# Optimization experiments

Measured on AMD Instinct MI355X. Metric: run time of the kernel, lower is better.

## Reference

```python
import jax, jax.numpy as jnp
import numpy as np

B, L, D, H, M = 2, 4096, 1024, 16, 256
DH = D // H
EPS = 1e-6
LN_EPS = 1e-5


def setup_inputs() -> dict:
    key = jax.random.key(0)
    ks = jax.random.split(key, 6)
    inp = {
        "x": jax.random.normal(ks[0], (B, L, D), jnp.float32),
        "Wq": jax.random.normal(ks[1], (D, D), jnp.float32) * (D ** -0.5),
        "Wk": jax.random.normal(ks[2], (D, D), jnp.float32) * (D ** -0.5),
        "Wv": jax.random.normal(ks[3], (D, D), jnp.float32) * (D ** -0.5),
        "Wo": jax.random.normal(ks[4], (D, D), jnp.float32) * (D ** -0.5),
        "proj": jax.random.normal(ks[5], (H, M, DH), jnp.float32),
        "ln_g": jnp.ones((D,), jnp.float32),
        "ln_b": jnp.zeros((D,), jnp.float32),
        "scale_factor": 2,
    }
    return inp


def _heads(t, W):
    b, l, _ = t.shape
    return (t @ W).reshape(b, l, H, DH).transpose(0, 2, 1, 3)  # bhld


def _favor_features(u, proj):
    # u: [B,H,L,DH] already scaled by d_head**-0.25; proj: [H,M,DH]
    dash = jnp.einsum("bhld,hmd->bhlm", u, proj)
    diag = 0.5 * jnp.sum(u * u, axis=-1, keepdims=True)  # [B,H,L,1]
    stab = jnp.max(dash, axis=-1, keepdims=True)
    return jnp.exp(dash - diag - stab) * (M ** -0.5)  # [B,H,L,M]


def reference(x, Wq, Wk, Wv, Wo, proj, ln_g, ln_b, scale_factor):
    b, l, d = x.shape
    # nearest-neighbor upsample along sequence (F.interpolate default mode)
    up = jnp.repeat(x, scale_factor, axis=1)  # [B, L*s, D]

    scale = DH ** -0.25
    q = _heads(up, Wq) * scale   # [B,H,Lq,DH]
    k = _heads(x, Wk) * scale    # [B,H,L,DH]
    v = _heads(x, Wv)            # [B,H,L,DH]

    qf = _favor_features(q, proj)  # [B,H,Lq,M]
    kf = _favor_features(k, proj)  # [B,H,L,M]

    kv = jnp.einsum("bhlm,bhld->bhmd", kf, v)          # [B,H,M,DH]
    k_sum = jnp.sum(kf, axis=2)                          # [B,H,M]
    z = 1.0 / (jnp.einsum("bhlm,bhm->bhl", qf, k_sum) + EPS)
    attn = jnp.einsum("bhlm,bhmd->bhld", qf, kv) * z[..., None]

    lq = attn.shape[2]
    y = attn.transpose(0, 2, 1, 3).reshape(b, lq, d) @ Wo
    y = jax.nn.gelu(y, approximate=False)

    mu = jnp.mean(y, axis=-1, keepdims=True)
    var = jnp.mean((y - mu) ** 2, axis=-1, keepdims=True)
    return (y - mu) * jax.lax.rsqrt(var + LN_EPS) * ln_g + ln_b
```

## Files before the change

### kernel.cpp

```cpp
#include <hip/hip_runtime.h>

static constexpr int kB  = 2;
static constexpr int kL  = 4096;
static constexpr int kD  = 1024;
static constexpr int kH  = 16;
static constexpr int kDH = 64;
static constexpr int kM  = 256;
static constexpr int kN  = kB * kL;
static constexpr float kScale    = 0.35355339059327373f;
static constexpr float kInvSqrtM = 0.0625f;
static constexpr float kEps   = 1e-6f;
static constexpr float kLnEps = 1e-5f;

typedef __attribute__((ext_vector_type(8))) short short8;
typedef __attribute__((ext_vector_type(4))) float f32x4;

__device__ __forceinline__ float bf2f(unsigned short h) {
  union { unsigned int u; float f; } c;
  c.u = ((unsigned int)h) << 16;
  return c.f;
}
__device__ __forceinline__ unsigned short f2bf(float f) {
  union { float f; unsigned int u; } c;
  c.f = f;
  unsigned int u = c.u;
  u += 0x7fffu + ((u >> 16) & 1u);
  return (unsigned short)(u >> 16);
}

__device__ __forceinline__ void gload_lds16(const unsigned short* g,
                                            unsigned short* l) {
  __builtin_amdgcn_global_load_lds(
      (const __attribute__((address_space(1))) unsigned int*)g,
      (__attribute__((address_space(3))) unsigned int*)l, 16, 0, 0);
}

__global__ __launch_bounds__(256) void cast_bf16_kernel(
    const float* __restrict__ in, unsigned short* __restrict__ out)
{
  const int i = blockIdx.x * 256 + threadIdx.x;
  float4 v = ((const float4*)in)[i];
  ushort4 o;
  o.x = f2bf(v.x); o.y = f2bf(v.y); o.z = f2bf(v.z); o.w = f2bf(v.w);
  ((ushort4*)out)[i] = o;
}

__global__ __launch_bounds__(256) void transpose_cast_kernel(
    const float* __restrict__ W, unsigned short* __restrict__ WT)
{
  __shared__ float tile[32][33];
  const int n0 = blockIdx.x * 32, k0 = blockIdx.y * 32;
  const int t = threadIdx.x, kk = t >> 5, nn = t & 31;
#pragma unroll
  for (int i = 0; i < 4; ++i)
    tile[kk + i * 8][nn] = W[(size_t)(k0 + kk + i * 8) * kD + n0 + nn];
  __syncthreads();
#pragma unroll
  for (int i = 0; i < 4; ++i)
    WT[(size_t)(n0 + kk + i * 8) * kD + k0 + nn] = f2bf(tile[nn][kk + i * 8]);
}

template <int OUT_MODE>
__global__ __launch_bounds__(256) void gemm_mfma(
    const unsigned short* __restrict__ A, const unsigned short* __restrict__ BT,
    void* __restrict__ Cout, float alpha)
{
  __shared__ unsigned short As[128 * 32];
  __shared__ unsigned short Bs[128 * 32];
  __shared__ unsigned short Tbuf[OUT_MODE == 2 ? 64 * 136 : 1];
  const int tid = threadIdx.x, lane = tid & 63, w = tid >> 6;
  const int q = lane >> 4, c = lane & 15;
  const int wr = (w >> 1) * 64, wc = (w & 1) * 64;
  const int row0 = blockIdx.y * 128, col0 = blockIdx.x * 128;
  const int lrow = lane >> 2, lcol = (lane & 3) * 8;

  f32x4 acc[4][4];
#pragma unroll
  for (int i = 0; i < 4; ++i)
#pragma unroll
    for (int j = 0; j < 4; ++j) acc[i][j] = (f32x4)0.f;

  for (int k0 = 0; k0 < kD; k0 += 32) {
#pragma unroll
    for (int i = 0; i < 2; ++i) {
      const int r0 = w * 32 + i * 16;
      gload_lds16(&A[(size_t)(row0 + r0 + lrow) * kD + k0 + lcol], &As[r0 * 32]);
      gload_lds16(&BT[(size_t)(col0 + r0 + lrow) * kD + k0 + lcol], &Bs[r0 * 32]);
    }
    __syncthreads();
    short8 av[4], bv[4];
#pragma unroll
    for (int i = 0; i < 4; ++i)
      av[i] = *(const short8*)&As[(wr + i * 16 + c) * 32 + q * 8];
#pragma unroll
    for (int j = 0; j < 4; ++j)
      bv[j] = *(const short8*)&Bs[(wc + j * 16 + c) * 32 + q * 8];
#pragma unroll
    for (int i = 0; i < 4; ++i)
#pragma unroll
      for (int j = 0; j < 4; ++j)
        acc[i][j] = __builtin_amdgcn_mfma_f32_16x16x32_bf16(
            av[i], bv[j], acc[i][j], 0, 0, 0);
    __syncthreads();
  }

  if (OUT_MODE != 2) {
#pragma unroll
    for (int i = 0; i < 4; ++i)
#pragma unroll
      for (int j = 0; j < 4; ++j)
#pragma unroll
        for (int r = 0; r < 4; ++r) {
          const int row = row0 + wr + i * 16 + q * 4 + r;
          const int col = col0 + wc + j * 16 + c;
          const float v = alpha * acc[i][j][r];
          if (OUT_MODE == 1)
            ((unsigned short*)Cout)[(size_t)row * kD + col] = f2bf(v);
          else
            ((float*)Cout)[(size_t)row * kD + col] = v;
        }
  } else {
    const int bq = row0 >> 12, l0 = row0 & 4095;
#pragma unroll
    for (int hh = 0; hh < 2; ++hh) {
      if ((w & 1) == hh) {
#pragma unroll
        for (int i = 0; i < 4; ++i)
#pragma unroll
          for (int j = 0; j < 4; ++j) {
            ushort4 o;
            o.x = f2bf(acc[i][j][0]); o.y = f2bf(acc[i][j][1]);
            o.z = f2bf(acc[i][j][2]); o.w = f2bf(acc[i][j][3]);
            *(ushort4*)&Tbuf[(j * 16 + c) * 136 + wr + i * 16 + q * 4] = o;
          }
      }
      __syncthreads();
      {
        const int dl = tid >> 2, seg = tid & 3;
        const size_t dst =
            ((size_t)(bq * 1024 + col0 + hh * 64 + dl)) * (size_t)kL +
            l0 + seg * 32;
        uint4* gp = (uint4*)((unsigned short*)Cout + dst);
        const unsigned short* sp = &Tbuf[dl * 136 + seg * 32];
#pragma unroll
        for (int u = 0; u < 4; ++u) gp[u] = *(const uint4*)&sp[u * 8];
      }
      __syncthreads();
    }
  }
}

template <int TRANS>
__global__ __launch_bounds__(256) void favor_mfma(
    const unsigned short* __restrict__ U, const unsigned short* __restrict__ projb,
    unsigned short* __restrict__ F)
{
  __shared__ unsigned short Us[128 * 72];
  __shared__ unsigned short Tbuf[TRANS ? 64 * 136 : 1];
  __shared__ float diagp[256];
  __shared__ float diag[128];
  const int bh = blockIdx.x, b = bh >> 4, h = bh & 15;
  const int l0 = blockIdx.y * 128;
  const int tid = threadIdx.x, lane = tid & 63, w = tid >> 6;
  const int q = lane >> 4, c = lane & 15;
  const int wr = w * 32;

#pragma unroll
  for (int it = 0; it < 4; ++it) {
    int idx = it * 256 + tid;
    int row = idx >> 3, col8 = idx & 7;
    *(uint4*)&Us[row * 72 + col8 * 8] =
        *(const uint4*)&U[((size_t)(b * kL + l0 + row)) * kD + h * kDH + col8 * 8];
  }
  __syncthreads();

  {
    int row = tid & 127, half = tid >> 7;
    const unsigned short* ur = &Us[row * 72 + half * 32];
    float s = 0.f;
#pragma unroll
    for (int d8 = 0; d8 < 4; ++d8) {
      uint4 raw = *(const uint4*)&ur[d8 * 8];
      const unsigned short* us = (const unsigned short*)&raw;
#pragma unroll
      for (int j = 0; j < 8; ++j) { float v = bf2f(us[j]); s = fmaf(v, v, s); }
    }
    diagp[half * 128 + row] = s;
  }

  f32x4 acc[2][16];
#pragma unroll
  for (int i = 0; i < 2; ++i)
#pragma unroll
    for (int j = 0; j < 16; ++j) acc[i][j] = (f32x4)0.f;

#pragma unroll
  for (int ks = 0; ks < 2; ++ks) {
    short8 av[2];
#pragma unroll
    for (int i = 0; i < 2; ++i)
      av[i] = *(const short8*)&Us[(wr + i * 16 + c) * 72 + ks * 32 + q * 8];
#pragma unroll
    for (int jb = 0; jb < 2; ++jb) {
      short8 bv[8];
#pragma unroll
      for (int jl = 0; jl < 8; ++jl)
        bv[jl] = *(const short8*)&projb[
            ((size_t)(h * kM + (jb * 8 + jl) * 16 + c)) * kDH + ks * 32 + q * 8];
#pragma unroll
      for (int jl = 0; jl < 8; ++jl)
#pragma unroll
        for (int i = 0; i < 2; ++i)
          acc[i][jb * 8 + jl] = __builtin_amdgcn_mfma_f32_16x16x32_bf16(
              av[i], bv[jl], acc[i][jb * 8 + jl], 0, 0, 0);
    }
  }

  __syncthreads();
  if (tid < 128) diag[tid] = 0.5f * (diagp[tid] + diagp[128 + tid]);
  __syncthreads();

#pragma unroll
  for (int i = 0; i < 2; ++i)
#pragma unroll
    for (int r = 0; r < 4; ++r) {
      const int lrow = wr + i * 16 + q * 4 + r;
      float mx = -3.4e38f;
#pragma unroll
      for (int j = 0; j < 16; ++j) mx = fmaxf(mx, acc[i][j][r]);
      mx = fmaxf(mx, __shfl_xor(mx, 1, 64));
      mx = fmaxf(mx, __shfl_xor(mx, 2, 64));
      mx = fmaxf(mx, __shfl_xor(mx, 4, 64));
      mx = fmaxf(mx, __shfl_xor(mx, 8, 64));
      const float base = diag[lrow] + mx;
      if (TRANS == 0) {
        const size_t gbase = ((size_t)bh * kL + (l0 + lrow)) * kM;
#pragma unroll
        for (int j = 0; j < 16; ++j)
          F[gbase + j * 16 + c] = f2bf(__expf(acc[i][j][r] - base) * kInvSqrtM);
      } else {
#pragma unroll
        for (int j = 0; j < 16; ++j)
          acc[i][j][r] = __expf(acc[i][j][r] - base) * kInvSqrtM;
      }
    }

  if (TRANS == 1) {
#pragma unroll
    for (int mc = 0; mc < 4; ++mc) {
      __syncthreads();
#pragma unroll
      for (int jl = 0; jl < 4; ++jl) {
        const int jj = mc * 4 + jl;
#pragma unroll
        for (int i = 0; i < 2; ++i) {
          ushort4 o;
          o.x = f2bf(acc[i][jj][0]); o.y = f2bf(acc[i][jj][1]);
          o.z = f2bf(acc[i][jj][2]); o.w = f2bf(acc[i][jj][3]);
          *(ushort4*)&Tbuf[(jl * 16 + c) * 136 + wr + i * 16 + q * 4] = o;
        }
      }
      __syncthreads();
#pragma unroll
      for (int it = 0; it < 4; ++it) {
        int idx = it * 256 + tid;
        int row = idx >> 4, col8 = idx & 15;
        *(uint4*)&F[((size_t)(bh * kM + mc * 64 + row)) * (size_t)kL +
                    l0 + col8 * 8] = *(const uint4*)&Tbuf[row * 136 + col8 * 8];
      }
    }
  }
}

__global__ __launch_bounds__(256) void kv_mfma(
    const unsigned short* __restrict__ KFT, const unsigned short* __restrict__ VT,
    float* __restrict__ KVP, float* __restrict__ KSP)
{
  __shared__ unsigned short As[128 * 40];
  __shared__ unsigned short Bs[64 * 40];
  const int bh = blockIdx.x, mtile = blockIdx.y, split = blockIdx.z;
  const int tid = threadIdx.x, lane = tid & 63, w = tid >> 6;
  const int q = lane >> 4, c = lane & 15;
  const int l0 = split * 512;
  const unsigned short* Abase = KFT + ((size_t)(bh * kM + mtile * 128)) * kL + l0;
  const unsigned short* Bbase = VT + ((size_t)(bh * kDH)) * kL + l0;

  f32x4 acc[2][4];
#pragma unroll
  for (int i = 0; i < 2; ++i)
#pragma unroll
    for (int j = 0; j < 4; ++j) acc[i][j] = (f32x4)0.f;
  float ksr[2] = {0.f, 0.f};

  for (int k0 = 0; k0 < 512; k0 += 32) {
    __syncthreads();
#pragma unroll
    for (int it = 0; it < 2; ++it) {
      int idx = it * 256 + tid;
      int row = idx >> 2, c8 = (idx & 3) * 8;
      *(uint4*)&As[row * 40 + c8] = *(const uint4*)&Abase[(size_t)row * kL + k0 + c8];
    }
    {
      int row = tid >> 2, c8 = (tid & 3) * 8;
      *(uint4*)&Bs[row * 40 + c8] = *(const uint4*)&Bbase[(size_t)row * kL + k0 + c8];
    }
    __syncthreads();
    short8 av[2], bv[4];
#pragma unroll
    for (int i = 0; i < 2; ++i) {
      av[i] = *(const short8*)&As[(w * 32 + i * 16 + c) * 40 + q * 8];
#pragma unroll
      for (int e = 0; e < 8; ++e) ksr[i] += bf2f((unsigned short)av[i][e]);
    }
#pragma unroll
    for (int j = 0; j < 4; ++j)
      bv[j] = *(const short8*)&Bs[(j * 16 + c) * 40 + q * 8];
#pragma unroll
    for (int i = 0; i < 2; ++i)
#pragma unroll
      for (int j = 0; j < 4; ++j)
        acc[i][j] = __builtin_amdgcn_mfma_f32_16x16x32_bf16(
            av[i], bv[j], acc[i][j], 0, 0, 0);
  }

  const int blk = (bh * 2 + mtile) * 8 + split;
  float* op = KVP + (size_t)blk * (128 * 64);
#pragma unroll
  for (int i = 0; i < 2; ++i)
#pragma unroll
    for (int j = 0; j < 4; ++j)
#pragma unroll
      for (int r = 0; r < 4; ++r)
        op[(w * 32 + i * 16 + q * 4 + r) * 64 + j * 16 + c] = acc[i][j][r];

#pragma unroll
  for (int i = 0; i < 2; ++i) {
    float s = ksr[i];
    s += __shfl_xor(s, 16, 64);
    s += __shfl_xor(s, 32, 64);
    if (q == 0) KSP[blk * 128 + w * 32 + i * 16 + c] = s;
  }
}

__global__ __launch_bounds__(256) void kv_reduce_kernel(
    const float* __restrict__ KVP, const float* __restrict__ KSP,
    unsigned short* __restrict__ KVT)
{
  const int blk = blockIdx.x;
  const int bh = blk / 80, n = blk - bh * 80;
  const int t = threadIdx.x;
  const int mt = t >> 7, ml = t & 127;
  float s = 0.f;
  if (n < 64) {
#pragma unroll
    for (int sp = 0; sp < 8; ++sp)
      s += KVP[((size_t)((bh * 2 + mt) * 8 + sp)) * (128 * 64) + ml * 64 + n];
  } else if (n == 64) {
#pragma unroll
    for (int sp = 0; sp < 8; ++sp)
      s += KSP[((bh * 2 + mt) * 8 + sp) * 128 + ml];
  }
  KVT[(size_t)bh * (80 * kM) + n * kM + t] = f2bf(s);
}

__global__ __launch_bounds__(256) void attn_mfma(
    const unsigned short* __restrict__ QF, const unsigned short* __restrict__ KVT,
    unsigned short* __restrict__ ATTN)
{
  __shared__ unsigned short kvs[80 * 264];
  __shared__ unsigned short qs[128 * 40];
  const int bh = blockIdx.x, b = bh >> 4, h = bh & 15;
  const int l0 = blockIdx.y * 128;
  const int tid = threadIdx.x, lane = tid & 63, w = tid >> 6;
  const int q = lane >> 4, c = lane & 15;
  const int trow = tid >> 2, tc8 = (tid & 3) * 8;

#pragma unroll
  for (int it = 0; it < 20; ++it) {
    int idx4 = it * 256 + tid;
    int row = idx4 >> 6, col4 = idx4 & 63;
    *(ushort4*)&kvs[row * 264 + col4 * 4] =
        *(const ushort4*)&KVT[(size_t)bh * (80 * kM) + row * kM + col4 * 4];
  }

  f32x4 acc[2][5];
#pragma unroll
  for (int i = 0; i < 2; ++i)
#pragma unroll
    for (int j = 0; j < 5; ++j) acc[i][j] = (f32x4)0.f;

  for (int kk = 0; kk < 8; ++kk) {
    __syncthreads();
#pragma unroll
    for (int i = 0; i < 2; ++i)
      *(uint4*)&qs[(trow + 64 * i) * 40 + tc8] =
          *(const uint4*)&QF[((size_t)bh * kL + (l0 + trow + 64 * i)) * kM +
                             kk * 32 + tc8];
    __syncthreads();
    short8 bv[5];
#pragma unroll
    for (int j = 0; j < 5; ++j)
      bv[j] = *(const short8*)&kvs[(j * 16 + c) * 264 + kk * 32 + q * 8];
#pragma unroll
    for (int i = 0; i < 2; ++i) {
      short8 av = *(const short8*)&qs[(w * 32 + i * 16 + c) * 40 + q * 8];
#pragma unroll
      for (int j = 0; j < 5; ++j)
        acc[i][j] = __builtin_amdgcn_mfma_f32_16x16x32_bf16(
            av, bv[j], acc[i][j], 0, 0, 0);
    }
  }

#pragma unroll
  for (int i = 0; i < 2; ++i)
#pragma unroll
    for (int r = 0; r < 4; ++r) {
      float den = __shfl(acc[i][4][r], (lane & 48));
      float z = 1.f / (den + kEps);
      const int row = l0 + w * 32 + i * 16 + q * 4 + r;
      const size_t base = ((size_t)(b * kL + row)) * kD + h * kDH;
#pragma unroll
      for (int j = 0; j < 4; ++j)
        ATTN[base + j * 16 + c] = f2bf(acc[i][j][r] * z);
    }
}

__global__ __launch_bounds__(256) void gelu_ln_kernel(
    const float* __restrict__ Y, const float* __restrict__ lng,
    const float* __restrict__ lnb, float* __restrict__ OUT)
{
  __shared__ float r1[4], r2[4];
  const int n = blockIdx.x;
  const int tid = threadIdx.x, lane = tid & 63, w = tid >> 6;

  float4 y4 = ((const float4*)(Y + (size_t)n * kD))[tid];
  float g0 = 0.5f * y4.x * (1.f + erff(y4.x * 0.70710678118654752f));
  float g1 = 0.5f * y4.y * (1.f + erff(y4.y * 0.70710678118654752f));
  float g2 = 0.5f * y4.z * (1.f + erff(y4.z * 0.70710678118654752f));
  float g3 = 0.5f * y4.w * (1.f + erff(y4.w * 0.70710678118654752f));

  float s  = (g0 + g1) + (g2 + g3);
  float ss = (g0 * g0 + g1 * g1) + (g2 * g2 + g3 * g3);
#pragma unroll
  for (int off = 32; off; off >>= 1) {
    s  += __shfl_xor(s, off, 64);
    ss += __shfl_xor(ss, off, 64);
  }
  if (lane == 0) { r1[w] = s; r2[w] = ss; }
  __syncthreads();
  s  = (r1[0] + r1[1]) + (r1[2] + r1[3]);
  ss = (r2[0] + r2[1]) + (r2[2] + r2[3]);
  float mu  = s * (1.f / (float)kD);
  float var = ss * (1.f / (float)kD) - mu * mu;
  float inv = rsqrtf(var + kLnEps);

  float4 gg = ((const float4*)lng)[tid];
  float4 bb = ((const float4*)lnb)[tid];
  float4 o;
  o.x = (g0 - mu) * inv * gg.x + bb.x;
  o.y = (g1 - mu) * inv * gg.y + bb.y;
  o.z = (g2 - mu) * inv * gg.z + bb.z;
  o.w = (g3 - mu) * inv * gg.w + bb.w;

  const int b = n >> 12, l = n & 4095;
  const int cc = tid * 4;
  size_t base = ((size_t)(b * 8192 + 2 * l)) * kD + cc;
  *(float4*)(OUT + base)      = o;
  *(float4*)(OUT + base + kD) = o;
}

extern "C" void kernel_launch(void* const* d_in, const int* in_sizes, int n_in,
                              void* d_out, int out_size, void* d_ws, size_t ws_size,
                              hipStream_t stream)
{
  (void)in_sizes; (void)n_in; (void)out_size; (void)ws_size;
  const float* x    = (const float*)d_in[0];
  const float* Wq   = (const float*)d_in[1];
  const float* Wk   = (const float*)d_in[2];
  const float* Wv   = (const float*)d_in[3];
  const float* Wo   = (const float*)d_in[4];
  const float* proj = (const float*)d_in[5];
  const float* lng  = (const float*)d_in[6];
  const float* lnb  = (const float*)d_in[7];
  float* out = (float*)d_out;

  char* ws = (char*)d_ws;
  const size_t MB = 1024 * 1024;
  unsigned short* xb  = (unsigned short*)(ws);
  unsigned short* WqT = (unsigned short*)(ws + 16 * MB);
  unsigned short* WkT = (unsigned short*)(ws + 18 * MB);
  unsigned short* WvT = (unsigned short*)(ws + 20 * MB);
  unsigned short* WoT = (unsigned short*)(ws + 22 * MB);
  unsigned short* Qb  = (unsigned short*)(ws + 24 * MB);
  unsigned short* Kb  = (unsigned short*)(ws + 40 * MB);
  unsigned short* VT  = (unsigned short*)(ws + 56 * MB);
  unsigned short* QF  = (unsigned short*)(ws + 72 * MB);
  unsigned short* KFT = (unsigned short*)(ws + 136 * MB);
  float* KSP          = (float*)(ws + 200 * MB);
  unsigned short* KVT = (unsigned short*)(ws + 201 * MB);
  unsigned short* projb = (unsigned short*)(ws + 203 * MB);
  float* KVP          = (float*)(ws + 24 * MB);
  unsigned short* ATTN = Kb;
  float* Y            = (float*)(ws + 72 * MB);

  cast_bf16_kernel<<<(kN * kD) / 1024, 256, 0, stream>>>(x, xb);
  cast_bf16_kernel<<<(kH * kM * kDH) / 1024, 256, 0, stream>>>(proj, projb);
  transpose_cast_kernel<<<dim3(32, 32), 256, 0, stream>>>(Wq, WqT);
  transpose_cast_kernel<<<dim3(32, 32), 256, 0, stream>>>(Wk, WkT);
  transpose_cast_kernel<<<dim3(32, 32), 256, 0, stream>>>(Wv, WvT);
  transpose_cast_kernel<<<dim3(32, 32), 256, 0, stream>>>(Wo, WoT);

  dim3 gg(8, 64);
  gemm_mfma<1><<<gg, 256, 0, stream>>>(xb, WkT, Kb, kScale);
  gemm_mfma<2><<<gg, 256, 0, stream>>>(xb, WvT, VT, 1.0f);
  gemm_mfma<1><<<gg, 256, 0, stream>>>(xb, WqT, Qb, kScale);

  favor_mfma<0><<<dim3(32, 32), 256, 0, stream>>>(Qb, projb, QF);
  favor_mfma<1><<<dim3(32, 32), 256, 0, stream>>>(Kb, projb, KFT);

  kv_mfma<<<dim3(32, 2, 8), 256, 0, stream>>>(KFT, VT, KVP, KSP);
  kv_reduce_kernel<<<32 * 80, 256, 0, stream>>>(KVP, KSP, KVT);

  attn_mfma<<<dim3(32, 32), 256, 0, stream>>>(QF, KVT, ATTN);

  gemm_mfma<0><<<gg, 256, 0, stream>>>(ATTN, WoT, Y, 1.0f);

  gelu_ln_kernel<<<kN, 256, 0, stream>>>(Y, lng, lnb, out);
}
```

Before: 389.4 us.

## Halve favor kernel row tile and drop LDS transpose for key features

The favor feature kernel now processes 64 rows per block instead of 128, so each wave holds one 16-row MFMA tile and half the accumulators, with a launch bound requesting higher occupancy and twice as many blocks. The transposed key-feature path no longer stages through an LDS buffer with extra barriers. It writes 4-element bf16 vectors straight to global memory in the transposed layout. This is meant to cut register pressure and barrier cost, at the price of narrower, less coalesced global stores and reloading projection rows for more blocks.

New measurement: 403.9 us. 1.04x slower.

```diff
diff --git a/kernel.cpp b/kernel.cpp
--- a/kernel.cpp
+++ b/kernel.cpp
@@ -151,22 +151,21 @@
 }
 
 template <int TRANS>
-__global__ __launch_bounds__(256) void favor_mfma(
+__global__ __launch_bounds__(256, 4) void favor_mfma(
     const unsigned short* __restrict__ U, const unsigned short* __restrict__ projb,
     unsigned short* __restrict__ F)
 {
-  __shared__ unsigned short Us[128 * 72];
-  __shared__ unsigned short Tbuf[TRANS ? 64 * 136 : 1];
-  __shared__ float diagp[256];
-  __shared__ float diag[128];
+  __shared__ unsigned short Us[64 * 72];
+  __shared__ float diagp[4][64];
+  __shared__ float diag[64];
   const int bh = blockIdx.x, b = bh >> 4, h = bh & 15;
-  const int l0 = blockIdx.y * 128;
+  const int l0 = blockIdx.y * 64;
   const int tid = threadIdx.x, lane = tid & 63, w = tid >> 6;
   const int q = lane >> 4, c = lane & 15;
-  const int wr = w * 32;
-
-#pragma unroll
-  for (int it = 0; it < 4; ++it) {
+  const int wrow = w * 16;
+
+#pragma unroll
+  for (int it = 0; it < 2; ++it) {
     int idx = it * 256 + tid;
     int row = idx >> 3, col8 = idx & 7;
     *(uint4*)&Us[row * 72 + col8 * 8] =
@@ -175,99 +174,77 @@
   __syncthreads();
 
   {
-    int row = tid & 127, half = tid >> 7;
-    const unsigned short* ur = &Us[row * 72 + half * 32];
+    int row = tid & 63, seg = tid >> 6;
+    const unsigned short* ur = &Us[row * 72 + seg * 16];
     float s = 0.f;
 #pragma unroll
-    for (int d8 = 0; d8 < 4; ++d8) {
+    for (int d8 = 0; d8 < 2; ++d8) {
       uint4 raw = *(const uint4*)&ur[d8 * 8];
       const unsigned short* us = (const unsigned short*)&raw;
 #pragma unroll
       for (int j = 0; j < 8; ++j) { float v = bf2f(us[j]); s = fmaf(v, v, s); }
     }
-    diagp[half * 128 + row] = s;
-  }
-
-  f32x4 acc[2][16];
-#pragma unroll
-  for (int i = 0; i < 2; ++i)
-#pragma unroll
-    for (int j = 0; j < 16; ++j) acc[i][j] = (f32x4)0.f;
+    diagp[seg][row] = s;
+  }
+  __syncthreads();
+  if (tid < 64)
+    diag[tid] = 0.5f * ((diagp[0][tid] + diagp[1][tid]) +
+                        (diagp[2][tid] + diagp[3][tid]));
+
+  f32x4 acc[16];
+#pragma unroll
+  for (int j = 0; j < 16; ++j) acc[j] = (f32x4)0.f;
 
 #pragma unroll
   for (int ks = 0; ks < 2; ++ks) {
-    short8 av[2];
-#pragma unroll
-    for (int i = 0; i < 2; ++i)
-      av[i] = *(const short8*)&Us[(wr + i * 16 + c) * 72 + ks * 32 + q * 8];
-#pragma unroll
-    for (int jb = 0; jb < 2; ++jb) {
-      short8 bv[8];
-#pragma unroll
-      for (int jl = 0; jl < 8; ++jl)
+    const short8 av = *(const short8*)&Us[(wrow + c) * 72 + ks * 32 + q * 8];
+#pragma unroll
+    for (int jb = 0; jb < 4; ++jb) {
+      short8 bv[4];
+#pragma unroll
+      for (int jl = 0; jl < 4; ++jl)
         bv[jl] = *(const short8*)&projb[
-            ((size_t)(h * kM + (jb * 8 + jl) * 16 + c)) * kDH + ks * 32 + q * 8];
-#pragma unroll
-      for (int jl = 0; jl < 8; ++jl)
-#pragma unroll
-        for (int i = 0; i < 2; ++i)
-          acc[i][jb * 8 + jl] = __builtin_amdgcn_mfma_f32_16x16x32_bf16(
-              av[i], bv[jl], acc[i][jb * 8 + jl], 0, 0, 0);
-    }
-  }
-
+            ((size_t)(h * kM + (jb * 4 + jl) * 16 + c)) * kDH + ks * 32 + q * 8];
+#pragma unroll
+      for (int jl = 0; jl < 4; ++jl)
+        acc[jb * 4 + jl] = __builtin_amdgcn_mfma_f32_16x16x32_bf16(
+            av, bv[jl], acc[jb * 4 + jl], 0, 0, 0);
+    }
+  }
   __syncthreads();
-  if (tid < 128) diag[tid] = 0.5f * (diagp[tid] + diagp[128 + tid]);
-  __syncthreads();
-
-#pragma unroll
-  for (int i = 0; i < 2; ++i)
+
+  float base_[4];
+#pragma unroll
+  for (int r = 0; r < 4; ++r) {
+    float mx = -3.4e38f;
+#pragma unroll
+    for (int j = 0; j < 16; ++j) mx = fmaxf(mx, acc[j][r]);
+    mx = fmaxf(mx, __shfl_xor(mx, 1, 64));
+    mx = fmaxf(mx, __shfl_xor(mx, 2, 64));
+    mx = fmaxf(mx, __shfl_xor(mx, 4, 64));
+    mx = fmaxf(mx, __shfl_xor(mx, 8, 64));
+    base_[r] = diag[wrow + q * 4 + r] + mx;
+  }
+
+  if (TRANS == 0) {
 #pragma unroll
     for (int r = 0; r < 4; ++r) {
-      const int lrow = wr + i * 16 + q * 4 + r;
-      float mx = -3.4e38f;
-#pragma unroll
-      for (int j = 0; j < 16; ++j) mx = fmaxf(mx, acc[i][j][r]);
-      mx = fmaxf(mx, __shfl_xor(mx, 1, 64));
-      mx = fmaxf(mx, __shfl_xor(mx, 2, 64));
-      mx = fmaxf(mx, __shfl_xor(mx, 4, 64));
-      mx = fmaxf(mx, __shfl_xor(mx, 8, 64));
-      const float base = diag[lrow] + mx;
-      if (TRANS == 0) {
-        const size_t gbase = ((size_t)bh * kL + (l0 + lrow)) * kM;
-#pragma unroll
-        for (int j = 0; j < 16; ++j)
-          F[gbase + j * 16 + c] = f2bf(__expf(acc[i][j][r] - base) * kInvSqrtM);
-      } else {
-#pragma unroll
-        for (int j = 0; j < 16; ++j)
-          acc[i][j][r] = __expf(acc[i][j][r] - base) * kInvSqrtM;
-      }
-    }
-
-  if (TRANS == 1) {
-#pragma unroll
-    for (int mc = 0; mc < 4; ++mc) {
-      __syncthreads();
-#pragma unroll
-      for (int jl = 0; jl < 4; ++jl) {
-        const int jj = mc * 4 + jl;
-#pragma unroll
-        for (int i = 0; i < 2; ++i) {
-          ushort4 o;
-          o.x = f2bf(acc[i][jj][0]); o.y = f2bf(acc[i][jj][1]);
-          o.z = f2bf(acc[i][jj][2]); o.w = f2bf(acc[i][jj][3]);
-          *(ushort4*)&Tbuf[(jl * 16 + c) * 136 + wr + i * 16 + q * 4] = o;
-        }
-      }
-      __syncthreads();
-#pragma unroll
-      for (int it = 0; it < 4; ++it) {
-        int idx = it * 256 + tid;
-        int row = idx >> 4, col8 = idx & 15;
-        *(uint4*)&F[((size_t)(bh * kM + mc * 64 + row)) * (size_t)kL +
-                    l0 + col8 * 8] = *(const uint4*)&Tbuf[row * 136 + col8 * 8];
-      }
+      const size_t gbase = ((size_t)bh * kL + (l0 + wrow + q * 4 + r)) * kM;
+#pragma unroll
+      for (int j = 0; j < 16; ++j)
+        F[gbase + j * 16 + c] =
+            f2bf(__expf(acc[j][r] - base_[r]) * kInvSqrtM);
+    }
+  } else {
+#pragma unroll
+    for (int j = 0; j < 16; ++j) {
+      ushort4 o;
+      o.x = f2bf(__expf(acc[j][0] - base_[0]) * kInvSqrtM);
+      o.y = f2bf(__expf(acc[j][1] - base_[1]) * kInvSqrtM);
+      o.z = f2bf(__expf(acc[j][2] - base_[2]) * kInvSqrtM);
+      o.w = f2bf(__expf(acc[j][3] - base_[3]) * kInvSqrtM);
+      *(ushort4*)&F[((size_t)(bh * kM + j * 16 + c)) * (size_t)kL +
+                    l0 + wrow + q * 4] = o;
     }
   }
 }
@@ -515,8 +492,8 @@
   gemm_mfma<2><<<gg, 256, 0, stream>>>(xb, WvT, VT, 1.0f);
   gemm_mfma<1><<<gg, 256, 0, stream>>>(xb, WqT, Qb, kScale);
 
-  favor_mfma<0><<<dim3(32, 32), 256, 0, stream>>>(Qb, projb, QF);
-  favor_mfma<1><<<dim3(32, 32), 256, 0, stream>>>(Kb, projb, KFT);
+  favor_mfma<0><<<dim3(32, 64), 256, 0, stream>>>(Qb, projb, QF);
+  favor_mfma<1><<<dim3(32, 64), 256, 0, stream>>>(Kb, projb, KFT);
 
   kv_mfma<<<dim3(32, 2, 8), 256, 0, stream>>>(KFT, VT, KVP, KSP);
   kv_reduce_kernel<<<32 * 80, 256, 0, stream>>>(KVP, KSP, KVT);
```

## Fuse query FAVOR feature computation into the attention kernel

Applied to the files above, without the earlier changes.

Query random features are now computed in LDS inside a new fused kernel that immediately multiplies them with the reduced KV/normalizer matrix. The large QF intermediate is no longer written to or read back from global memory. The key-side favor kernel becomes a dedicated transposed-output version, and launches are reordered with the workspace offsets compacted. The fused kernel reads KVT directly from global/L2 rather than staging it in LDS, and uses smaller 64-row tiles.

After: 387.9 us. About the same (-0.4%).

```diff
diff --git a/kernel.cpp b/kernel.cpp
--- a/kernel.cpp
+++ b/kernel.cpp
@@ -150,13 +150,12 @@
   }
 }
 
-template <int TRANS>
-__global__ __launch_bounds__(256) void favor_mfma(
+__global__ __launch_bounds__(256) void favor_k_mfma(
     const unsigned short* __restrict__ U, const unsigned short* __restrict__ projb,
     unsigned short* __restrict__ F)
 {
   __shared__ unsigned short Us[128 * 72];
-  __shared__ unsigned short Tbuf[TRANS ? 64 * 136 : 1];
+  __shared__ unsigned short Tbuf[64 * 136];
   __shared__ float diagp[256];
   __shared__ float diag[128];
   const int bh = blockIdx.x, b = bh >> 4, h = bh & 15;
@@ -233,42 +232,160 @@
       mx = fmaxf(mx, __shfl_xor(mx, 4, 64));
       mx = fmaxf(mx, __shfl_xor(mx, 8, 64));
       const float base = diag[lrow] + mx;
-      if (TRANS == 0) {
-        const size_t gbase = ((size_t)bh * kL + (l0 + lrow)) * kM;
-#pragma unroll
-        for (int j = 0; j < 16; ++j)
-          F[gbase + j * 16 + c] = f2bf(__expf(acc[i][j][r] - base) * kInvSqrtM);
-      } else {
-#pragma unroll
-        for (int j = 0; j < 16; ++j)
-          acc[i][j][r] = __expf(acc[i][j][r] - base) * kInvSqrtM;
+#pragma unroll
+      for (int j = 0; j < 16; ++j)
+        acc[i][j][r] = __expf(acc[i][j][r] - base) * kInvSqrtM;
+    }
+
+#pragma unroll
+  for (int mc = 0; mc < 4; ++mc) {
+    __syncthreads();
+#pragma unroll
+    for (int jl = 0; jl < 4; ++jl) {
+      const int jj = mc * 4 + jl;
+#pragma unroll
+      for (int i = 0; i < 2; ++i) {
+        ushort4 o;
+        o.x = f2bf(acc[i][jj][0]); o.y = f2bf(acc[i][jj][1]);
+        o.z = f2bf(acc[i][jj][2]); o.w = f2bf(acc[i][jj][3]);
+        *(ushort4*)&Tbuf[(jl * 16 + c) * 136 + wr + i * 16 + q * 4] = o;
       }
     }
-
-  if (TRANS == 1) {
-#pragma unroll
-    for (int mc = 0; mc < 4; ++mc) {
-      __syncthreads();
-#pragma unroll
-      for (int jl = 0; jl < 4; ++jl) {
-        const int jj = mc * 4 + jl;
-#pragma unroll
-        for (int i = 0; i < 2; ++i) {
-          ushort4 o;
-          o.x = f2bf(acc[i][jj][0]); o.y = f2bf(acc[i][jj][1]);
-          o.z = f2bf(acc[i][jj][2]); o.w = f2bf(acc[i][jj][3]);
-          *(ushort4*)&Tbuf[(jl * 16 + c) * 136 + wr + i * 16 + q * 4] = o;
-        }
-      }
-      __syncthreads();
-#pragma unroll
-      for (int it = 0; it < 4; ++it) {
-        int idx = it * 256 + tid;
-        int row = idx >> 4, col8 = idx & 15;
-        *(uint4*)&F[((size_t)(bh * kM + mc * 64 + row)) * (size_t)kL +
-                    l0 + col8 * 8] = *(const uint4*)&Tbuf[row * 136 + col8 * 8];
-      }
-    }
+    __syncthreads();
+#pragma unroll
+    for (int it = 0; it < 4; ++it) {
+      int idx = it * 256 + tid;
+      int row = idx >> 4, col8 = idx & 15;
+      *(uint4*)&F[((size_t)(bh * kM + mc * 64 + row)) * (size_t)kL +
+                  l0 + col8 * 8] = *(const uint4*)&Tbuf[row * 136 + col8 * 8];
+    }
+  }
+}
+
+__global__ __launch_bounds__(256, 3) void fused_qattn(
+    const unsigned short* __restrict__ Qb, const unsigned short* __restrict__ projb,
+    const unsigned short* __restrict__ KVT, unsigned short* __restrict__ ATTN)
+{
+  __shared__ unsigned short qs[64 * 72];
+  __shared__ unsigned short qfs[64 * 264];
+  __shared__ float diagp[4][64];
+  __shared__ float maxp[4][64];
+  __shared__ float basev[64];
+  const int bh = blockIdx.x, b = bh >> 4, h = bh & 15;
+  const int l0 = blockIdx.y * 64;
+  const int tid = threadIdx.x, lane = tid & 63, w = tid >> 6;
+  const int q = lane >> 4, c = lane & 15;
+
+#pragma unroll
+  for (int it = 0; it < 2; ++it) {
+    int idx = it * 256 + tid;
+    int row = idx >> 3, col8 = idx & 7;
+    *(uint4*)&qs[row * 72 + col8 * 8] =
+        *(const uint4*)&Qb[((size_t)(b * kL + l0 + row)) * kD + h * kDH + col8 * 8];
+  }
+  __syncthreads();
+
+  {
+    int row = tid & 63, seg = tid >> 6;
+    const unsigned short* ur = &qs[row * 72 + seg * 16];
+    float s = 0.f;
+#pragma unroll
+    for (int d8 = 0; d8 < 2; ++d8) {
+      uint4 raw = *(const uint4*)&ur[d8 * 8];
+      const unsigned short* us = (const unsigned short*)&raw;
+#pragma unroll
+      for (int j = 0; j < 8; ++j) { float v = bf2f(us[j]); s = fmaf(v, v, s); }
+    }
+    diagp[seg][row] = s;
+  }
+
+  f32x4 acc[4][4];
+#pragma unroll
+  for (int i = 0; i < 4; ++i)
+#pragma unroll
+    for (int j = 0; j < 4; ++j) acc[i][j] = (f32x4)0.f;
+
+#pragma unroll
+  for (int ks = 0; ks < 2; ++ks) {
+    short8 av[4], bv[4];
+#pragma unroll
+    for (int i = 0; i < 4; ++i)
+      av[i] = *(const short8*)&projb[
+          ((size_t)(h * kM + w * 64 + i * 16 + c)) * kDH + ks * 32 + q * 8];
+#pragma unroll
+    for (int j = 0; j < 4; ++j)
+      bv[j] = *(const short8*)&qs[(j * 16 + c) * 72 + ks * 32 + q * 8];
+#pragma unroll
+    for (int i = 0; i < 4; ++i)
+#pragma unroll
+      for (int j = 0; j < 4; ++j)
+        acc[i][j] = __builtin_amdgcn_mfma_f32_16x16x32_bf16(
+            av[i], bv[j], acc[i][j], 0, 0, 0);
+  }
+
+#pragma unroll
+  for (int j = 0; j < 4; ++j) {
+    float mx = -3.4e38f;
+#pragma unroll
+    for (int i = 0; i < 4; ++i)
+#pragma unroll
+      for (int r = 0; r < 4; ++r) mx = fmaxf(mx, acc[i][j][r]);
+    mx = fmaxf(mx, __shfl_xor(mx, 16, 64));
+    mx = fmaxf(mx, __shfl_xor(mx, 32, 64));
+    if (q == 0) maxp[w][j * 16 + c] = mx;
+  }
+  __syncthreads();
+  if (tid < 64) {
+    float d = 0.5f * ((diagp[0][tid] + diagp[1][tid]) +
+                      (diagp[2][tid] + diagp[3][tid]));
+    float m4 = fmaxf(fmaxf(maxp[0][tid], maxp[1][tid]),
+                     fmaxf(maxp[2][tid], maxp[3][tid]));
+    basev[tid] = d + m4;
+  }
+  __syncthreads();
+
+#pragma unroll
+  for (int j = 0; j < 4; ++j) {
+    const float bs = basev[j * 16 + c];
+#pragma unroll
+    for (int i = 0; i < 4; ++i) {
+      ushort4 o;
+      o.x = f2bf(__expf(acc[i][j][0] - bs) * kInvSqrtM);
+      o.y = f2bf(__expf(acc[i][j][1] - bs) * kInvSqrtM);
+      o.z = f2bf(__expf(acc[i][j][2] - bs) * kInvSqrtM);
+      o.w = f2bf(__expf(acc[i][j][3] - bs) * kInvSqrtM);
+      *(ushort4*)&qfs[(j * 16 + c) * 264 + w * 64 + i * 16 + q * 4] = o;
+    }
+  }
+  __syncthreads();
+
+  f32x4 acc2[5];
+#pragma unroll
+  for (int j = 0; j < 5; ++j) acc2[j] = (f32x4)0.f;
+
+#pragma unroll
+  for (int kk = 0; kk < 8; ++kk) {
+    short8 av2 = *(const short8*)&qfs[(w * 16 + c) * 264 + kk * 32 + q * 8];
+    short8 bv2[5];
+#pragma unroll
+    for (int j = 0; j < 5; ++j)
+      bv2[j] = *(const short8*)&KVT[
+          (size_t)bh * (80 * kM) + (j * 16 + c) * kM + kk * 32 + q * 8];
+#pragma unroll
+    for (int j = 0; j < 5; ++j)
+      acc2[j] = __builtin_amdgcn_mfma_f32_16x16x32_bf16(
+          av2, bv2[j], acc2[j], 0, 0, 0);
+  }
+
+#pragma unroll
+  for (int r = 0; r < 4; ++r) {
+    float den = __shfl(acc2[4][r], (lane & 48));
+    float z = 1.f / (den + kEps);
+    const int row = l0 + w * 16 + q * 4 + r;
+    const size_t base = ((size_t)(b * kL + row)) * kD + h * kDH;
+#pragma unroll
+    for (int j = 0; j < 4; ++j)
+      ATTN[base + j * 16 + c] = f2bf(acc2[j][r] * z);
   }
 }
 
@@ -361,68 +478,6 @@
       s += KSP[((bh * 2 + mt) * 8 + sp) * 128 + ml];
   }
   KVT[(size_t)bh * (80 * kM) + n * kM + t] = f2bf(s);
-}
-
-__global__ __launch_bounds__(256) void attn_mfma(
-    const unsigned short* __restrict__ QF, const unsigned short* __restrict__ KVT,
-    unsigned short* __restrict__ ATTN)
-{
-  __shared__ unsigned short kvs[80 * 264];
-  __shared__ unsigned short qs[128 * 40];
-  const int bh = blockIdx.x, b = bh >> 4, h = bh & 15;
-  const int l0 = blockIdx.y * 128;
-  const int tid = threadIdx.x, lane = tid & 63, w = tid >> 6;
-  const int q = lane >> 4, c = lane & 15;
-  const int trow = tid >> 2, tc8 = (tid & 3) * 8;
-
-#pragma unroll
-  for (int it = 0; it < 20; ++it) {
-    int idx4 = it * 256 + tid;
-    int row = idx4 >> 6, col4 = idx4 & 63;
-    *(ushort4*)&kvs[row * 264 + col4 * 4] =
-        *(const ushort4*)&KVT[(size_t)bh * (80 * kM) + row * kM + col4 * 4];
-  }
-
-  f32x4 acc[2][5];
-#pragma unroll
-  for (int i = 0; i < 2; ++i)
-#pragma unroll
-    for (int j = 0; j < 5; ++j) acc[i][j] = (f32x4)0.f;
-
-  for (int kk = 0; kk < 8; ++kk) {
-    __syncthreads();
-#pragma unroll
-    for (int i = 0; i < 2; ++i)
-      *(uint4*)&qs[(trow + 64 * i) * 40 + tc8] =
-          *(const uint4*)&QF[((size_t)bh * kL + (l0 + trow + 64 * i)) * kM +
-                             kk * 32 + tc8];
-    __syncthreads();
-    short8 bv[5];
-#pragma unroll
-    for (int j = 0; j < 5; ++j)
-      bv[j] = *(const short8*)&kvs[(j * 16 + c) * 264 + kk * 32 + q * 8];
-#pragma unroll
-    for (int i = 0; i < 2; ++i) {
-      short8 av = *(const short8*)&qs[(w * 32 + i * 16 + c) * 40 + q * 8];
-#pragma unroll
-      for (int j = 0; j < 5; ++j)
-        acc[i][j] = __builtin_amdgcn_mfma_f32_16x16x32_bf16(
-            av, bv[j], acc[i][j], 0, 0, 0);
-    }
-  }
-
-#pragma unroll
-  for (int i = 0; i < 2; ++i)
-#pragma unroll
-    for (int r = 0; r < 4; ++r) {
-      float den = __shfl(acc[i][4][r], (lane & 48));
-      float z = 1.f / (den + kEps);
-      const int row = l0 + w * 32 + i * 16 + q * 4 + r;
-      const size_t base = ((size_t)(b * kL + row)) * kD + h * kDH;
-#pragma unroll
-      for (int j = 0; j < 4; ++j)
-        ATTN[base + j * 16 + c] = f2bf(acc[i][j][r] * z);
-    }
 }
 
 __global__ __launch_bounds__(256) void gelu_ln_kernel(
@@ -494,12 +549,11 @@
   unsigned short* Qb  = (unsigned short*)(ws + 24 * MB);
   unsigned short* Kb  = (unsigned short*)(ws + 40 * MB);
   unsigned short* VT  = (unsigned short*)(ws + 56 * MB);
-  unsigned short* QF  = (unsigned short*)(ws + 72 * MB);
-  unsigned short* KFT = (unsigned short*)(ws + 136 * MB);
-  float* KSP          = (float*)(ws + 200 * MB);
-  unsigned short* KVT = (unsigned short*)(ws + 201 * MB);
-  unsigned short* projb = (unsigned short*)(ws + 203 * MB);
-  float* KVP          = (float*)(ws + 24 * MB);
+  unsigned short* KFT = (unsigned short*)(ws + 72 * MB);
+  float* KVP          = (float*)(ws + 136 * MB);
+  float* KSP          = (float*)(ws + 152 * MB);
+  unsigned short* KVT = (unsigned short*)(ws + 153 * MB);
+  unsigned short* projb = (unsigned short*)(ws + 155 * MB);
   unsigned short* ATTN = Kb;
   float* Y            = (float*)(ws + 72 * MB);
 
@@ -512,16 +566,13 @@
 
   dim3 gg(8, 64);
   gemm_mfma<1><<<gg, 256, 0, stream>>>(xb, WkT, Kb, kScale);
+  favor_k_mfma<<<dim3(32, 32), 256, 0, stream>>>(Kb, projb, KFT);
   gemm_mfma<2><<<gg, 256, 0, stream>>>(xb, WvT, VT, 1.0f);
-  gemm_mfma<1><<<gg, 256, 0, stream>>>(xb, WqT, Qb, kScale);
-
-  favor_mfma<0><<<dim3(32, 32), 256, 0, stream>>>(Qb, projb, QF);
-  favor_mfma<1><<<dim3(32, 32), 256, 0, stream>>>(Kb, projb, KFT);
-
   kv_mfma<<<dim3(32, 2, 8), 256, 0, stream>>>(KFT, VT, KVP, KSP);
   kv_reduce_kernel<<<32 * 80, 256, 0, stream>>>(KVP, KSP, KVT);
 
-  attn_mfma<<<dim3(32, 32), 256, 0, stream>>>(QF, KVT, ATTN);
+  gemm_mfma<1><<<gg, 256, 0, stream>>>(xb, WqT, Qb, kScale);
+  fused_qattn<<<dim3(32, 64), 256, 0, stream>>>(Qb, projb, KVT, ATTN);
 
   gemm_mfma<0><<<gg, 256, 0, stream>>>(ATTN, WoT, Y, 1.0f);
 
```
